# Kernel optimization log

Hardware: AMD Instinct MI355X
Metric: run time of the kernel (lower is better)

The kernel has to match this reference:

```python
import jax, jax.numpy as jnp
import numpy as np

HIDDEN = 2048
N_HEADS = 16
HEAD_DIM = HIDDEN // N_HEADS
MAX_POS = 4096
ROPE_THETA = 10000.0
B, S = 2, 4096


def rotate_half(x):
    d = x.shape[-1] // 2
    return jnp.concatenate([-x[..., d:], x[..., :d]], axis=-1)


def make_rope_cache(seq_len, dim, base):
    inv_freq = 1.0 / (base ** (np.arange(0, dim, 2, dtype=np.float32) / dim))
    t = np.arange(seq_len, dtype=np.float32)
    freqs = np.einsum('i,j->ij', t, inv_freq)
    emb = np.concatenate([freqs, freqs], axis=-1)
    return jnp.asarray(np.cos(emb)), jnp.asarray(np.sin(emb))


def setup_inputs() -> dict:
    key = jax.random.key(0)
    k1, k2, k3, k4, k5, k6 = jax.random.split(key, 6)
    hidden_states = jax.random.normal(k1, (B, S, HIDDEN), dtype=jnp.float32)
    # causal additive mask [B,1,S,S]
    causal = jnp.where(jnp.tril(jnp.ones((S, S), dtype=bool)), 0.0, -1e9).astype(jnp.float32)
    attention_mask = jnp.broadcast_to(causal[None, None], (B, 1, S, S))
    position_ids = jnp.broadcast_to(jnp.arange(S, dtype=jnp.int64)[None], (B, S))
    scale = 0.02
    Wq = jax.random.normal(k2, (HIDDEN, HIDDEN), dtype=jnp.float32) * scale
    Wk = jax.random.normal(k3, (HIDDEN, HIDDEN), dtype=jnp.float32) * scale
    Wv = jax.random.normal(k4, (HIDDEN, HIDDEN), dtype=jnp.float32) * scale
    Wo = jax.random.normal(k5, (HIDDEN, HIDDEN), dtype=jnp.float32) * scale
    return {"hidden_states": hidden_states, "attention_mask": attention_mask,
            "position_ids": position_ids, "Wq": Wq, "Wk": Wk, "Wv": Wv, "Wo": Wo}


def reference(hidden_states, attention_mask, position_ids, Wq, Wk, Wv, Wo):
    bsz, q_len, _ = hidden_states.shape
    # projections (torch Linear: x @ W.T; here W stored as [in,out] -> x @ W)
    q = (hidden_states @ Wq).reshape(bsz, q_len, N_HEADS, HEAD_DIM).transpose(0, 2, 1, 3)
    k = (hidden_states @ Wk).reshape(bsz, q_len, N_HEADS, HEAD_DIM).transpose(0, 2, 1, 3)
    v = (hidden_states @ Wv).reshape(bsz, q_len, N_HEADS, HEAD_DIM).transpose(0, 2, 1, 3)
    cos_c, sin_c = make_rope_cache(q_len, HEAD_DIM, ROPE_THETA)
    cos = cos_c[position_ids][:, None]  # [B,1,S,Dh]
    sin = sin_c[position_ids][:, None]
    q = q * cos + rotate_half(q) * sin
    k = k * cos + rotate_half(k) * sin
    scores = jnp.einsum('bhqd,bhkd->bhqk', q, k) / jnp.sqrt(jnp.float32(HEAD_DIM))
    scores = scores + attention_mask
    probs = jax.nn.softmax(scores.astype(jnp.float32), axis=-1).astype(q.dtype)
    attn = jnp.einsum('bhqk,bhkd->bhqd', probs, v)
    attn = attn.transpose(0, 2, 1, 3).reshape(bsz, q_len, HIDDEN)
    return attn @ Wo
```

## Files before the change

### kernel.cpp

```cpp
#include <hip/hip_runtime.h>

#define HID 2048
#define NHEADS 16
#define DHEAD 128
#define BB 2
#define SS 4096
#define MTOT (BB * SS)

typedef __attribute__((ext_vector_type(8))) short short8;
typedef __attribute__((ext_vector_type(8))) unsigned short ushort8;
typedef __attribute__((ext_vector_type(4))) float floatx4;
typedef __attribute__((ext_vector_type(16))) float floatx16;

static __device__ __forceinline__ ushort f2bf(float f) {
  unsigned x = __float_as_uint(f);
  return (ushort)((x + 0x7fffu + ((x >> 16) & 1u)) >> 16);
}
static __device__ __forceinline__ float bf2f(ushort u) {
  return __uint_as_float(((unsigned)u) << 16);
}
static __device__ __forceinline__ unsigned cvtpk_bf16(float lo, float hi) {
  unsigned r;
  asm("v_cvt_pk_bf16_f32 %0, %1, %2" : "=v"(r) : "v"(lo), "v"(hi));
  return r;
}
static __device__ __forceinline__ void pl32swap(unsigned& a, unsigned& b) {
  asm volatile("v_permlane32_swap_b32 %0, %1" : "+v"(a), "+v"(b));
}
static __device__ __forceinline__ floatx16 fz16() {
  floatx16 z;
#pragma unroll
  for (int i = 0; i < 16; i++) z[i] = 0.f;
  return z;
}

#define GL16(g, l)                                                   \
  __builtin_amdgcn_global_load_lds(                                  \
      (const __attribute__((address_space(1))) unsigned int*)(g),    \
      (__attribute__((address_space(3))) unsigned int*)(l), 16, 0, 0)

__global__ void k_cvt_bf16(const float* __restrict__ x, ushort* __restrict__ o, int n4) {
  int i = blockIdx.x * blockDim.x + threadIdx.x;
  int stride = gridDim.x * blockDim.x;
  for (; i < n4; i += stride) {
    float4 v = reinterpret_cast<const float4*>(x)[i];
    ushort4 u;
    u.x = f2bf(v.x); u.y = f2bf(v.y); u.z = f2bf(v.z); u.w = f2bf(v.w);
    reinterpret_cast<ushort4*>(o)[i] = u;
  }
}

__global__ __launch_bounds__(256) void k_wt(const float* __restrict__ W, ushort* __restrict__ Wt) {
  __shared__ float tile[64][65];
  int n0 = blockIdx.x * 64, k0 = blockIdx.y * 64;
  int t = threadIdx.x;
#pragma unroll
  for (int i = 0; i < 16; i++) {
    int idx = t + i * 256, r = idx >> 6, c = idx & 63;
    tile[r][c] = W[(size_t)(k0 + r) * HID + n0 + c];
  }
  __syncthreads();
#pragma unroll
  for (int i = 0; i < 16; i++) {
    int idx = t + i * 256, r = idx >> 6, c = idx & 63;
    Wt[(size_t)(n0 + r) * HID + k0 + c] = f2bf(tile[c][r]);
  }
}

__global__ void k_rope_tab(float* __restrict__ cosT, float* __restrict__ sinT) {
  int idx = blockIdx.x * 256 + threadIdx.x;
  int pos = idx >> 6, j = idx & 63;
  float inv = powf(10000.0f, -(float)(2 * j) * (1.0f / 128.0f));
  float a = (float)pos * inv;
  cosT[idx] = cosf(a);
  sinT[idx] = sinf(a);
}

__global__ void k_rope(ushort* __restrict__ Q, ushort* __restrict__ Kb,
                       const float* __restrict__ cosT, const float* __restrict__ sinT) {
  const float kSc = 0.12751742f;
  int idx = blockIdx.x * 256 + threadIdx.x;
  int j4 = (idx & 15) * 4;
  int hh = (idx >> 4) & (NHEADS - 1);
  int srow = idx >> 8;
  int pos = srow & (SS - 1);
  float4 c = *reinterpret_cast<const float4*>(&cosT[pos * 64 + j4]);
  float4 s = *reinterpret_cast<const float4*>(&sinT[pos * 64 + j4]);
  size_t base = (size_t)srow * HID + hh * DHEAD + j4;
  ushort4 qa = *reinterpret_cast<ushort4*>(&Q[base]);
  ushort4 qb = *reinterpret_cast<ushort4*>(&Q[base + 64]);
  ushort4 ka = *reinterpret_cast<ushort4*>(&Kb[base]);
  ushort4 kb = *reinterpret_cast<ushort4*>(&Kb[base + 64]);
  ushort4 o1, o2, o3, o4;
  float cc[4] = {c.x, c.y, c.z, c.w}, ss[4] = {s.x, s.y, s.z, s.w};
  ushort* pqa = &qa.x; ushort* pqb = &qb.x; ushort* pka = &ka.x; ushort* pkb = &kb.x;
  ushort* po1 = &o1.x; ushort* po2 = &o2.x; ushort* po3 = &o3.x; ushort* po4 = &o4.x;
#pragma unroll
  for (int i = 0; i < 4; i++) {
    float a1 = bf2f(pqa[i]), a2 = bf2f(pqb[i]);
    po1[i] = f2bf((a1 * cc[i] - a2 * ss[i]) * kSc);
    po2[i] = f2bf((a2 * cc[i] + a1 * ss[i]) * kSc);
    float b1 = bf2f(pka[i]), b2 = bf2f(pkb[i]);
    po3[i] = f2bf(b1 * cc[i] - b2 * ss[i]);
    po4[i] = f2bf(b2 * cc[i] + b1 * ss[i]);
  }
  *reinterpret_cast<ushort4*>(&Q[base]) = o1;
  *reinterpret_cast<ushort4*>(&Q[base + 64]) = o2;
  *reinterpret_cast<ushort4*>(&Kb[base]) = o3;
  *reinterpret_cast<ushort4*>(&Kb[base + 64]) = o4;
}

template <int OUT_BF16>
__global__ __launch_bounds__(512, 2) void k_gemm8(const ushort* __restrict__ A,
                                                  const ushort* __restrict__ Bt,
                                                  void* __restrict__ Cp,
                                                  int Mr, int Nc, int Kd) {
  __shared__ ushort As[2][256 * 64];
  __shared__ ushort Bs[2][256 * 64];
  int t = threadIdx.x;
  int lane = t & 63, wid = t >> 6;
  int lrow = lane & 15, lk = lane >> 4;
  int wr = wid >> 2, wc = wid & 3;

  int nbx = Nc >> 8;
  int nwg = gridDim.x;
  int cpx = nwg >> 3;
  int id = blockIdx.x;
  int swz = (id & 7) * cpx + (id >> 3);
  int m0 = (swz / nbx) << 8, n0 = (swz % nbx) << 8;

  floatx4 acc[8][4];
#pragma unroll
  for (int i = 0; i < 8; i++)
#pragma unroll
    for (int j = 0; j < 4; j++) acc[i][j] = (floatx4){0.f, 0.f, 0.f, 0.f};

  int srow = t >> 3;
  int sk = ((t & 7) ^ (srow & 7)) << 3;
  const ushort* gA = A + (size_t)(m0 + srow) * Kd + sk;
  const ushort* gB = Bt + (size_t)(n0 + srow) * Kd + sk;

  auto STAGE_A = [&](int buf, int kt) {
    const ushort* s = gA + kt * 64;
#pragma unroll
    for (int i = 0; i < 4; i++)
      GL16(s + (size_t)i * 64 * Kd, (char*)As + buf * 32768 + t * 16 + i * 8192);
  };
  auto STAGE_B = [&](int buf, int kt) {
    const ushort* s = gB + kt * 64;
#pragma unroll
    for (int i = 0; i < 4; i++)
      GL16(s + (size_t)i * 64 * Kd, (char*)Bs + buf * 32768 + t * 16 + i * 8192);
  };

  STAGE_A(0, 0);
  STAGE_B(0, 0);
  __syncthreads();

  int swzb = (lrow & 7) << 4;
  int nk = Kd >> 6;
  for (int tK = 0; tK < nk; ++tK) {
    int cur = tK & 1;
    bool pre = (tK + 1 < nk);
    const char* Ab_ = (const char*)As + cur * 32768;
    const char* Bb_ = (const char*)Bs + cur * 32768;
#pragma unroll
    for (int p = 0; p < 4; p++) {
      int mh = p >> 1, nh = p & 1;
      short8 af[4][2], bfr[2][2];
#pragma unroll
      for (int fm = 0; fm < 4; fm++) {
        int row = wr * 128 + mh * 64 + fm * 16 + lrow;
#pragma unroll
        for (int kk = 0; kk < 2; kk++)
          af[fm][kk] = *reinterpret_cast<const short8*>(
              Ab_ + ((row * 128 + kk * 64 + lk * 16) ^ swzb));
      }
#pragma unroll
      for (int fn = 0; fn < 2; fn++) {
        int row = wc * 64 + nh * 32 + fn * 16 + lrow;
#pragma unroll
        for (int kk = 0; kk < 2; kk++)
          bfr[fn][kk] = *reinterpret_cast<const short8*>(
              Bb_ + ((row * 128 + kk * 64 + lk * 16) ^ swzb));
      }
      if (pre) {
        if (p == 0) STAGE_A(cur ^ 1, tK + 1);
        if (p == 1) STAGE_B(cur ^ 1, tK + 1);
      }
      __builtin_amdgcn_sched_barrier(0);
      __builtin_amdgcn_s_barrier();
      __builtin_amdgcn_s_setprio(1);
#pragma unroll
      for (int kk = 0; kk < 2; kk++)
#pragma unroll
        for (int fm = 0; fm < 4; fm++)
#pragma unroll
          for (int fn = 0; fn < 2; fn++)
            acc[mh * 4 + fm][nh * 2 + fn] = __builtin_amdgcn_mfma_f32_16x16x32_bf16(
                af[fm][kk], bfr[fn][kk], acc[mh * 4 + fm][nh * 2 + fn], 0, 0, 0);
      __builtin_amdgcn_s_setprio(0);
      __builtin_amdgcn_sched_barrier(0);
      if (p == 3)
        __syncthreads();
      else
        __builtin_amdgcn_s_barrier();
    }
  }

#pragma unroll
  for (int am = 0; am < 8; am++)
#pragma unroll
    for (int an = 0; an < 4; an++)
#pragma unroll
      for (int r = 0; r < 4; r++) {
        int m = m0 + wr * 128 + (am >> 2) * 64 + (am & 3) * 16 + lk * 4 + r;
        int n = n0 + wc * 64 + (an >> 1) * 32 + (an & 1) * 16 + lrow;
        if (OUT_BF16)
          ((ushort*)Cp)[(size_t)m * Nc + n] = f2bf(acc[am][an][r]);
        else
          ((float*)Cp)[(size_t)m * Nc + n] = acc[am][an][r];
      }
}

__global__ __launch_bounds__(512, 2) void k_fattn(const ushort* __restrict__ Qg,
                                                  const ushort* __restrict__ Kg,
                                                  const ushort* __restrict__ Vt2,
                                                  ushort* __restrict__ Og) {
  __shared__ ushort Ks[2][64 * 128];
  __shared__ ushort Vs[2][128 * 64];
  int t = threadIdx.x, lane = t & 63, wid = t >> 6;
  int l31 = lane & 31, hi = lane >> 5;
  int pi = blockIdx.x, h = blockIdx.y, b = blockIdx.z;

  auto STAGE = [&](int buf, int kt) {
    int kv0 = kt * 64;
    const ushort* Kbase = Kg + (size_t)(b * SS + kv0) * HID + h * DHEAD;
    const ushort* Vbase = Vt2 + (size_t)(h * DHEAD) * MTOT + b * SS + kv0;
#pragma unroll
    for (int i = 0; i < 2; i++) {
      int L = t + i * 512;
      int row = L >> 4, cr = L & 15;
      GL16(Kbase + (size_t)row * HID + ((cr ^ (row & 7)) << 3),
           (char*)Ks + buf * 16384 + L * 16);
    }
#pragma unroll
    for (int i = 0; i < 2; i++) {
      int L = t + i * 512;
      int row = L >> 3, cr = L & 7;
      GL16(Vbase + (size_t)row * MTOT + ((cr ^ (row & 7)) << 3),
           (char*)Vs + buf * 16384 + L * 16);
    }
  };

  for (int e = 0; e < 2; e++) {
    int qt = e ? (15 - pi) : pi;
    int q0 = qt * 256;
    int wq0 = q0 + wid * 32;
    int qlane = wq0 + l31;

    short8 qf[8];
    {
      const ushort* qb = Qg + (size_t)(b * SS + qlane) * HID + h * DHEAD + hi * 8;
#pragma unroll
      for (int ks = 0; ks < 8; ks++)
        qf[ks] = *reinterpret_cast<const short8*>(qb + ks * 16);
    }

    floatx16 accO[4];
#pragma unroll
    for (int db = 0; db < 4; db++) accO[db] = fz16();
    float mrow = -1e30f, lsum = 0.f;

    int nkt = (qt + 1) * 4;
    __syncthreads();
    STAGE(0, 0);
    __syncthreads();

    for (int kt = 0; kt < nkt; kt++) {
      int cur = kt & 1;
      int kv0 = kt * 64;
      if (kt + 1 < nkt) STAGE(cur ^ 1, kt + 1);

      if (kv0 <= wq0 + 31) {
        const char* Kb_ = (const char*)Ks + cur * 16384;
        floatx16 accS[2];
        accS[0] = fz16(); accS[1] = fz16();
#pragma unroll
        for (int ks = 0; ks < 8; ks++) {
#pragma unroll
          for (int kvb = 0; kvb < 2; kvb++) {
            int row = kvb * 32 + l31;
            int byte_ = (row * 256 + ks * 32 + hi * 16) ^ ((row & 7) << 4);
            short8 kf = *reinterpret_cast<const short8*>(Kb_ + byte_);
            accS[kvb] = __builtin_amdgcn_mfma_f32_32x32x16_bf16(kf, qf[ks], accS[kvb], 0, 0, 0);
          }
        }

        if (kv0 + 63 > wq0) {
          int kvbase = kv0 + hi * 4;
#pragma unroll
          for (int kvb = 0; kvb < 2; kvb++)
#pragma unroll
            for (int r = 0; r < 16; r++) {
              int kvi = kvbase + kvb * 32 + (r & 3) + 8 * (r >> 2);
              if (kvi > qlane) accS[kvb][r] = -1e30f;
            }
        }

        float mA = -1e30f, mB = -1e30f, mC = -1e30f, mD = -1e30f;
#pragma unroll
        for (int r = 0; r < 16; r += 4) {
          mA = fmaxf(mA, fmaxf(accS[0][r], accS[1][r]));
          mB = fmaxf(mB, fmaxf(accS[0][r + 1], accS[1][r + 1]));
          mC = fmaxf(mC, fmaxf(accS[0][r + 2], accS[1][r + 2]));
          mD = fmaxf(mD, fmaxf(accS[0][r + 3], accS[1][r + 3]));
        }
        float mx = fmaxf(fmaxf(mA, mB), fmaxf(mC, mD));
        mx = fmaxf(mx, __shfl_xor(mx, 32));
        if (!__all(mx <= mrow + 8.0f)) {
          float mnew = fmaxf(mrow, mx);
          float corr = exp2f(mrow - mnew);
          mrow = mnew;
          lsum *= corr;
#pragma unroll
          for (int db = 0; db < 4; db++)
#pragma unroll
            for (int r = 0; r < 16; r++) accO[db][r] *= corr;
        }

        float sA = 0.f, sB = 0.f, sC = 0.f, sD = 0.f;
#pragma unroll
        for (int kvb = 0; kvb < 2; kvb++)
#pragma unroll
          for (int r = 0; r < 16; r += 4) {
            float p0 = exp2f(accS[kvb][r] - mrow);
            float p1 = exp2f(accS[kvb][r + 1] - mrow);
            float p2 = exp2f(accS[kvb][r + 2] - mrow);
            float p3 = exp2f(accS[kvb][r + 3] - mrow);
            accS[kvb][r] = p0; accS[kvb][r + 1] = p1;
            accS[kvb][r + 2] = p2; accS[kvb][r + 3] = p3;
            sA += p0; sB += p1; sC += p2; sD += p3;
          }
        lsum += ((sA + sB) + (sC + sD));

        const char* Vb_ = (const char*)Vs + cur * 16384;
#pragma unroll
        for (int ks = 0; ks < 4; ks++) {
          int kvb = ks >> 1, tt = ks & 1;
          unsigned w0 = cvtpk_bf16(accS[kvb][8 * tt + 0], accS[kvb][8 * tt + 1]);
          unsigned w2 = cvtpk_bf16(accS[kvb][8 * tt + 4], accS[kvb][8 * tt + 5]);
          pl32swap(w0, w2);
          unsigned w1 = cvtpk_bf16(accS[kvb][8 * tt + 2], accS[kvb][8 * tt + 3]);
          unsigned w3 = cvtpk_bf16(accS[kvb][8 * tt + 6], accS[kvb][8 * tt + 7]);
          pl32swap(w1, w3);
          union { unsigned u[4]; short8 v; } pf;
          pf.u[0] = w0; pf.u[1] = w1; pf.u[2] = w2; pf.u[3] = w3;
#pragma unroll
          for (int db = 0; db < 4; db++) {
            int row = db * 32 + l31;
            int byte_ = (row * 128 + ks * 32 + hi * 16) ^ ((row & 7) << 4);
            short8 vf = *reinterpret_cast<const short8*>(Vb_ + byte_);
            accO[db] = __builtin_amdgcn_mfma_f32_32x32x16_bf16(vf, pf.v, accO[db], 0, 0, 0);
          }
        }
      }
      __syncthreads();
    }

    float lt = lsum + __shfl_xor(lsum, 32);
    float inv = 1.0f / lt;
    __syncthreads();
    char* sb = ((wid < 4) ? (char*)Ks : (char*)Vs) + (wid & 3) * 8192;
#pragma unroll
    for (int db = 0; db < 4; db++)
#pragma unroll
      for (int r = 0; r < 16; r += 2) {
        int d = db * 32 + (r & 3) + 8 * (r >> 2) + hi * 4;
        unsigned w = cvtpk_bf16(accO[db][r] * inv, accO[db][r + 1] * inv);
        int byte_ = (l31 * 256 + d * 2) ^ ((l31 & 7) << 4);
        *reinterpret_cast<unsigned*>(sb + byte_) = w;
      }
#pragma unroll
    for (int i = 0; i < 8; i++) {
      int row = i * 4 + (lane >> 4);
      int byte_ = (row * 256 + (lane & 15) * 16) ^ ((row & 7) << 4);
      ushort8 ov = *reinterpret_cast<const ushort8*>(sb + byte_);
      *reinterpret_cast<ushort8*>(Og + (size_t)(b * SS + wq0 + row) * HID + h * DHEAD +
                                  (lane & 15) * 8) = ov;
    }
  }
}

extern "C" void kernel_launch(void* const* d_in, const int* in_sizes, int n_in,
                              void* d_out, int out_size, void* d_ws, size_t ws_size,
                              hipStream_t stream) {
  const float* X = (const float*)d_in[0];
  const float* Wq = (const float*)d_in[3];
  const float* Wk = (const float*)d_in[4];
  const float* Wv = (const float*)d_in[5];
  const float* Wo = (const float*)d_in[6];
  float* out = (float*)d_out;

  char* p = (char*)d_ws;
  const size_t szXb = (size_t)MTOT * HID * 2;
  const size_t szW = (size_t)HID * HID * 2;
  ushort* Xb = (ushort*)p;  p += szXb;
  ushort* Wqt = (ushort*)p; p += szW;
  ushort* Wkt = (ushort*)p; p += szW;
  ushort* Wvt = (ushort*)p; p += szW;
  ushort* Wot = (ushort*)p; p += szW;
  ushort* Qb = (ushort*)p;  p += szXb;
  ushort* Kb = (ushort*)p;  p += szXb;
  ushort* Vt2 = (ushort*)p; p += szXb;
  ushort* Ab = (ushort*)p;  p += szXb;
  float* cosT = (float*)p;  p += (size_t)SS * 64 * 4;
  float* sinT = (float*)p;  p += (size_t)SS * 64 * 4;

  k_cvt_bf16<<<2048, 256, 0, stream>>>(X, Xb, MTOT * HID / 4);
  dim3 wg(32, 32);
  k_wt<<<wg, 256, 0, stream>>>(Wq, Wqt);
  k_wt<<<wg, 256, 0, stream>>>(Wk, Wkt);
  k_wt<<<wg, 256, 0, stream>>>(Wv, Wvt);
  k_wt<<<wg, 256, 0, stream>>>(Wo, Wot);
  k_rope_tab<<<SS * 64 / 256, 256, 0, stream>>>(cosT, sinT);

  int gqk = (MTOT / 256) * (HID / 256);
  k_gemm8<1><<<gqk, 512, 0, stream>>>(Xb, Wqt, Qb, MTOT, HID, HID);
  k_gemm8<1><<<gqk, 512, 0, stream>>>(Xb, Wkt, Kb, MTOT, HID, HID);
  int gv = (HID / 256) * (MTOT / 256);
  k_gemm8<1><<<gv, 512, 0, stream>>>(Wvt, Xb, Vt2, HID, MTOT, HID);

  k_rope<<<MTOT * NHEADS * 16 / 256, 256, 0, stream>>>(Qb, Kb, cosT, sinT);

  dim3 ag(8, NHEADS, BB);
  k_fattn<<<ag, 512, 0, stream>>>(Qb, Kb, Vt2, Ab);

  k_gemm8<0><<<gqk, 512, 0, stream>>>(Ab, Wot, out, MTOT, HID, HID);
}
```

Measured before the change: 561.5 us.

## Triple-buffer K/V tiles and software-pipeline QK^T of next tile with softmax-PV

Moves the flash-attention KV loop from a double buffer to a triple-buffered LDS ring, prefetching two tiles ahead, and uses explicit vmcnt waits with raw s_barrier in place of __syncthreads. It also software-pipelines the loop so the QK^T MFMAs for tile kt+1 are issued before the softmax and PV work of tile kt, letting matrix-core work overlap with the exp and max VALU work. In exchange LDS per block grows to 96KB, which may limit occupancy at launch_bounds(512,2). The hand-written waitcnt and barrier scheduling also risks races if the vmcnt counts are wrong.

```diff
diff --git a/kernel.cpp b/kernel.cpp
--- a/kernel.cpp
+++ b/kernel.cpp
@@ -227,8 +227,7 @@
                                                   const ushort* __restrict__ Kg,
                                                   const ushort* __restrict__ Vt2,
                                                   ushort* __restrict__ Og) {
-  __shared__ ushort Ks[2][64 * 128];
-  __shared__ ushort Vs[2][128 * 64];
+  __shared__ __align__(16) char lds_[3 * 32768];
   int t = threadIdx.x, lane = t & 63, wid = t >> 6;
   int l31 = lane & 31, hi = lane >> 5;
   int pi = blockIdx.x, h = blockIdx.y, b = blockIdx.z;
@@ -237,19 +236,19 @@
     int kv0 = kt * 64;
     const ushort* Kbase = Kg + (size_t)(b * SS + kv0) * HID + h * DHEAD;
     const ushort* Vbase = Vt2 + (size_t)(h * DHEAD) * MTOT + b * SS + kv0;
+    char* kb = lds_ + buf * 32768;
+    char* vb = kb + 16384;
 #pragma unroll
     for (int i = 0; i < 2; i++) {
       int L = t + i * 512;
       int row = L >> 4, cr = L & 15;
-      GL16(Kbase + (size_t)row * HID + ((cr ^ (row & 7)) << 3),
-           (char*)Ks + buf * 16384 + L * 16);
+      GL16(Kbase + (size_t)row * HID + ((cr ^ (row & 7)) << 3), kb + L * 16);
     }
 #pragma unroll
     for (int i = 0; i < 2; i++) {
       int L = t + i * 512;
       int row = L >> 3, cr = L & 7;
-      GL16(Vbase + (size_t)row * MTOT + ((cr ^ (row & 7)) << 3),
-           (char*)Vs + buf * 16384 + L * 16);
+      GL16(Vbase + (size_t)row * MTOT + ((cr ^ (row & 7)) << 3), vb + L * 16);
     }
   };
 
@@ -271,107 +270,132 @@
 #pragma unroll
     for (int db = 0; db < 4; db++) accO[db] = fz16();
     float mrow = -1e30f, lsum = 0.f;
-
     int nkt = (qt + 1) * 4;
-    __syncthreads();
+
+    auto QKT = [&](int kt, int buf, floatx16& s0, floatx16& s1) {
+      const char* Kb_ = lds_ + buf * 32768;
+      s0 = fz16(); s1 = fz16();
+#pragma unroll
+      for (int ks = 0; ks < 8; ks++) {
+        {
+          int row = l31;
+          int byte_ = (row * 256 + ks * 32 + hi * 16) ^ ((row & 7) << 4);
+          short8 kf = *reinterpret_cast<const short8*>(Kb_ + byte_);
+          s0 = __builtin_amdgcn_mfma_f32_32x32x16_bf16(kf, qf[ks], s0, 0, 0, 0);
+        }
+        {
+          int row = 32 + l31;
+          int byte_ = (row * 256 + ks * 32 + hi * 16) ^ ((row & 7) << 4);
+          short8 kf = *reinterpret_cast<const short8*>(Kb_ + byte_);
+          s1 = __builtin_amdgcn_mfma_f32_32x32x16_bf16(kf, qf[ks], s1, 0, 0, 0);
+        }
+      }
+    };
+
+    auto SMPV = [&](int kt, floatx16& s0, floatx16& s1) {
+      int kv0 = kt * 64;
+      if (kv0 + 63 > wq0) {
+        int kvbase = kv0 + hi * 4;
+#pragma unroll
+        for (int r = 0; r < 16; r++) {
+          int kvi = kvbase + (r & 3) + 8 * (r >> 2);
+          if (kvi > qlane) s0[r] = -1e30f;
+          if (kvi + 32 > qlane) s1[r] = -1e30f;
+        }
+      }
+      float mA = -1e30f, mB = -1e30f, mC = -1e30f, mD = -1e30f;
+#pragma unroll
+      for (int r = 0; r < 16; r += 4) {
+        mA = fmaxf(mA, fmaxf(s0[r], s1[r]));
+        mB = fmaxf(mB, fmaxf(s0[r + 1], s1[r + 1]));
+        mC = fmaxf(mC, fmaxf(s0[r + 2], s1[r + 2]));
+        mD = fmaxf(mD, fmaxf(s0[r + 3], s1[r + 3]));
+      }
+      float mx = fmaxf(fmaxf(mA, mB), fmaxf(mC, mD));
+      mx = fmaxf(mx, __shfl_xor(mx, 32));
+      if (!__all(mx <= mrow + 8.0f)) {
+        float mnew = fmaxf(mrow, mx);
+        float corr = exp2f(mrow - mnew);
+        mrow = mnew;
+        lsum *= corr;
+#pragma unroll
+        for (int db = 0; db < 4; db++)
+#pragma unroll
+          for (int r = 0; r < 16; r++) accO[db][r] *= corr;
+      }
+      float sA = 0.f, sB = 0.f, sC = 0.f, sD = 0.f;
+#pragma unroll
+      for (int r = 0; r < 16; r += 4) {
+        float p0 = exp2f(s0[r] - mrow), q0_ = exp2f(s1[r] - mrow);
+        float p1 = exp2f(s0[r + 1] - mrow), q1_ = exp2f(s1[r + 1] - mrow);
+        float p2 = exp2f(s0[r + 2] - mrow), q2_ = exp2f(s1[r + 2] - mrow);
+        float p3 = exp2f(s0[r + 3] - mrow), q3_ = exp2f(s1[r + 3] - mrow);
+        s0[r] = p0; s1[r] = q0_; s0[r + 1] = p1; s1[r + 1] = q1_;
+        s0[r + 2] = p2; s1[r + 2] = q2_; s0[r + 3] = p3; s1[r + 3] = q3_;
+        sA += p0 + q0_; sB += p1 + q1_; sC += p2 + q2_; sD += p3 + q3_;
+      }
+      lsum += ((sA + sB) + (sC + sD));
+      const char* Vb_ = lds_ + (kt % 3) * 32768 + 16384;
+#pragma unroll
+      for (int ks = 0; ks < 4; ks++) {
+        int tt = ks & 1;
+        floatx16& sv = (ks < 2) ? s0 : s1;
+        unsigned w0 = cvtpk_bf16(sv[8 * tt + 0], sv[8 * tt + 1]);
+        unsigned w2 = cvtpk_bf16(sv[8 * tt + 4], sv[8 * tt + 5]);
+        pl32swap(w0, w2);
+        unsigned w1 = cvtpk_bf16(sv[8 * tt + 2], sv[8 * tt + 3]);
+        unsigned w3 = cvtpk_bf16(sv[8 * tt + 6], sv[8 * tt + 7]);
+        pl32swap(w1, w3);
+        union { unsigned u[4]; short8 v; } pf;
+        pf.u[0] = w0; pf.u[1] = w1; pf.u[2] = w2; pf.u[3] = w3;
+#pragma unroll
+        for (int db = 0; db < 4; db++) {
+          int row = db * 32 + l31;
+          int byte_ = (row * 128 + ks * 32 + hi * 16) ^ ((row & 7) << 4);
+          short8 vf = *reinterpret_cast<const short8*>(Vb_ + byte_);
+          accO[db] = __builtin_amdgcn_mfma_f32_32x32x16_bf16(vf, pf.v, accO[db], 0, 0, 0);
+        }
+      }
+    };
+
+    auto STEP = [&](int kt, floatx16& c0, floatx16& c1, floatx16& n0, floatx16& n1) {
+      bool haveNext = (kt + 1 < nkt);
+      if (kt + 2 < nkt) STAGE((kt + 2) % 3, kt + 2);
+      if (haveNext) {
+        if (kt + 2 < nkt)
+          asm volatile("s_waitcnt vmcnt(4)" ::: "memory");
+        else
+          asm volatile("s_waitcnt vmcnt(0)" ::: "memory");
+        __builtin_amdgcn_s_barrier();
+        asm volatile("" ::: "memory");
+        __builtin_amdgcn_sched_barrier(0);
+        if ((kt + 1) * 64 <= wq0 + 31)
+          QKT(kt + 1, (kt + 1) % 3, n0, n1);
+      }
+      if (kt * 64 <= wq0 + 31) SMPV(kt, c0, c1);
+      asm volatile("s_waitcnt lgkmcnt(0)" ::: "memory");
+      __builtin_amdgcn_s_barrier();
+      asm volatile("" ::: "memory");
+    };
+
+    __builtin_amdgcn_sched_barrier(0);
     STAGE(0, 0);
-    __syncthreads();
-
-    for (int kt = 0; kt < nkt; kt++) {
-      int cur = kt & 1;
-      int kv0 = kt * 64;
-      if (kt + 1 < nkt) STAGE(cur ^ 1, kt + 1);
-
-      if (kv0 <= wq0 + 31) {
-        const char* Kb_ = (const char*)Ks + cur * 16384;
-        floatx16 accS[2];
-        accS[0] = fz16(); accS[1] = fz16();
-#pragma unroll
-        for (int ks = 0; ks < 8; ks++) {
-#pragma unroll
-          for (int kvb = 0; kvb < 2; kvb++) {
-            int row = kvb * 32 + l31;
-            int byte_ = (row * 256 + ks * 32 + hi * 16) ^ ((row & 7) << 4);
-            short8 kf = *reinterpret_cast<const short8*>(Kb_ + byte_);
-            accS[kvb] = __builtin_amdgcn_mfma_f32_32x32x16_bf16(kf, qf[ks], accS[kvb], 0, 0, 0);
-          }
-        }
-
-        if (kv0 + 63 > wq0) {
-          int kvbase = kv0 + hi * 4;
-#pragma unroll
-          for (int kvb = 0; kvb < 2; kvb++)
-#pragma unroll
-            for (int r = 0; r < 16; r++) {
-              int kvi = kvbase + kvb * 32 + (r & 3) + 8 * (r >> 2);
-              if (kvi > qlane) accS[kvb][r] = -1e30f;
-            }
-        }
-
-        float mA = -1e30f, mB = -1e30f, mC = -1e30f, mD = -1e30f;
-#pragma unroll
-        for (int r = 0; r < 16; r += 4) {
-          mA = fmaxf(mA, fmaxf(accS[0][r], accS[1][r]));
-          mB = fmaxf(mB, fmaxf(accS[0][r + 1], accS[1][r + 1]));
-          mC = fmaxf(mC, fmaxf(accS[0][r + 2], accS[1][r + 2]));
-          mD = fmaxf(mD, fmaxf(accS[0][r + 3], accS[1][r + 3]));
-        }
-        float mx = fmaxf(fmaxf(mA, mB), fmaxf(mC, mD));
-        mx = fmaxf(mx, __shfl_xor(mx, 32));
-        if (!__all(mx <= mrow + 8.0f)) {
-          float mnew = fmaxf(mrow, mx);
-          float corr = exp2f(mrow - mnew);
-          mrow = mnew;
-          lsum *= corr;
-#pragma unroll
-          for (int db = 0; db < 4; db++)
-#pragma unroll
-            for (int r = 0; r < 16; r++) accO[db][r] *= corr;
-        }
-
-        float sA = 0.f, sB = 0.f, sC = 0.f, sD = 0.f;
-#pragma unroll
-        for (int kvb = 0; kvb < 2; kvb++)
-#pragma unroll
-          for (int r = 0; r < 16; r += 4) {
-            float p0 = exp2f(accS[kvb][r] - mrow);
-            float p1 = exp2f(accS[kvb][r + 1] - mrow);
-            float p2 = exp2f(accS[kvb][r + 2] - mrow);
-            float p3 = exp2f(accS[kvb][r + 3] - mrow);
-            accS[kvb][r] = p0; accS[kvb][r + 1] = p1;
-            accS[kvb][r + 2] = p2; accS[kvb][r + 3] = p3;
-            sA += p0; sB += p1; sC += p2; sD += p3;
-          }
-        lsum += ((sA + sB) + (sC + sD));
-
-        const char* Vb_ = (const char*)Vs + cur * 16384;
-#pragma unroll
-        for (int ks = 0; ks < 4; ks++) {
-          int kvb = ks >> 1, tt = ks & 1;
-          unsigned w0 = cvtpk_bf16(accS[kvb][8 * tt + 0], accS[kvb][8 * tt + 1]);
-          unsigned w2 = cvtpk_bf16(accS[kvb][8 * tt + 4], accS[kvb][8 * tt + 5]);
-          pl32swap(w0, w2);
-          unsigned w1 = cvtpk_bf16(accS[kvb][8 * tt + 2], accS[kvb][8 * tt + 3]);
-          unsigned w3 = cvtpk_bf16(accS[kvb][8 * tt + 6], accS[kvb][8 * tt + 7]);
-          pl32swap(w1, w3);
-          union { unsigned u[4]; short8 v; } pf;
-          pf.u[0] = w0; pf.u[1] = w1; pf.u[2] = w2; pf.u[3] = w3;
-#pragma unroll
-          for (int db = 0; db < 4; db++) {
-            int row = db * 32 + l31;
-            int byte_ = (row * 128 + ks * 32 + hi * 16) ^ ((row & 7) << 4);
-            short8 vf = *reinterpret_cast<const short8*>(Vb_ + byte_);
-            accO[db] = __builtin_amdgcn_mfma_f32_32x32x16_bf16(vf, pf.v, accO[db], 0, 0, 0);
-          }
-        }
-      }
-      __syncthreads();
+    STAGE(1, 1);
+    asm volatile("s_waitcnt vmcnt(4)" ::: "memory");
+    __builtin_amdgcn_s_barrier();
+    asm volatile("" ::: "memory");
+    __builtin_amdgcn_sched_barrier(0);
+
+    floatx16 sE0, sE1, sO0, sO1;
+    QKT(0, 0, sE0, sE1);
+    for (int kt = 0; kt < nkt; kt += 2) {
+      STEP(kt, sE0, sE1, sO0, sO1);
+      STEP(kt + 1, sO0, sO1, sE0, sE1);
     }
 
     float lt = lsum + __shfl_xor(lsum, 32);
     float inv = 1.0f / lt;
-    __syncthreads();
-    char* sb = ((wid < 4) ? (char*)Ks : (char*)Vs) + (wid & 3) * 8192;
+    char* sb = lds_ + wid * 8192;
 #pragma unroll
     for (int db = 0; db < 4; db++)
 #pragma unroll
@@ -389,6 +413,7 @@
       *reinterpret_cast<ushort8*>(Og + (size_t)(b * SS + wq0 + row) * HID + h * DHEAD +
                                   (lane & 15) * 8) = ov;
     }
+    __syncthreads();
   }
 }
 
```

Result: slower. 636.2 us (+13.3%).
